# Performance work log

Measured on AMD Instinct MI355X. Metric: run time of the kernel, lower is better.

## Reference

```python
import jax, jax.numpy as jnp
import numpy as np

B, S, I, H = 64, 2048, 128, 256


def setup_inputs() -> dict:
    key = jax.random.key(0)
    ks = jax.random.split(key, 14)
    std = 1.0 / np.sqrt(H)
    def mat(k, shape):
        # xavier-normal-ish init (exact distribution irrelevant for correctness)
        fan_in, fan_out = shape
        s = np.sqrt(2.0 / (fan_in + fan_out))
        return jax.random.normal(k, shape, dtype=jnp.float32) * s
    def vec(k):
        return jax.random.uniform(k, (H,), dtype=jnp.float32, minval=-std, maxval=std)
    return {
        "x": jax.random.normal(ks[0], (B, S, I), dtype=jnp.float32),
        "U_f": mat(ks[1], (I, H)), "W_f": mat(ks[2], (H, H)), "b_f": vec(ks[3]),
        "U_i": mat(ks[4], (I, H)), "W_i": mat(ks[5], (H, H)), "b_i": vec(ks[6]),
        "U_o": mat(ks[7], (I, H)), "W_o": mat(ks[8], (H, H)), "b_o": vec(ks[9]),
        "U_c": mat(ks[10], (I, H)), "W_c": mat(ks[11], (H, H)), "b_c": vec(ks[12]),
    }


def _lstm(x, U_f, W_f, b_f, U_i, W_i, b_i, U_o, W_o, b_o, U_c, W_c, b_c):
    batch, seq, _ = x.shape
    hid = W_f.shape[0]
    # Fuse the 4 input projections into one GEMM over the whole sequence (same math).
    U = jnp.concatenate([U_f, U_i, U_o, U_c], axis=1)           # [I, 4H]
    W = jnp.concatenate([W_f, W_i, W_o, W_c], axis=1)           # [H, 4H]
    b = jnp.concatenate([b_f, b_i, b_o, b_c], axis=0)           # [4H]
    xg = jnp.einsum('bsi,ig->sbg', x, U) + b                    # [S, B, 4H]

    def step(carry, xg_t):
        h, c = carry
        g = xg_t + h @ W                                         # [B, 4H]
        f_t = jax.nn.sigmoid(g[:, 0 * hid:1 * hid])
        i_t = jax.nn.sigmoid(g[:, 1 * hid:2 * hid])
        o_t = jax.nn.sigmoid(g[:, 2 * hid:3 * hid])
        # NOTE: source uses sigmoid (not tanh) for the candidate cell
        c_tilde = jax.nn.sigmoid(g[:, 3 * hid:4 * hid])
        c_new = f_t * c + i_t * c_tilde
        h_new = o_t * jnp.tanh(c_new)
        return (h_new, c_new), h_new

    h0 = jnp.zeros((batch, hid), dtype=x.dtype)
    c0 = jnp.zeros((batch, hid), dtype=x.dtype)
    (h_T, c_T), hs = jax.lax.scan(step, (h0, c0), xg)
    hidden_seq = jnp.transpose(hs, (1, 0, 2))                    # [B, S, H]
    return hidden_seq, (h_T, c_T)


def reference(x, U_f, W_f, b_f, U_i, W_i, b_i, U_o, W_o, b_o, U_c, W_c, b_c):
    return _lstm(x, U_f, W_f, b_f, U_i, W_i, b_i, U_o, W_o, b_o, U_c, W_c, b_c)
```

## Files before the change

### kernel.cpp

```cpp
#include <hip/hip_runtime.h>
#include <stdint.h>

typedef unsigned short ushort_t;
typedef unsigned int uint32;

#define SEQ   2048
#define BATCH 64
#define INDIM 128
#define HID   256
#define NGRP  4
#define NWGG  16
#define HSZ   (BATCH*SEQ*HID)

typedef __attribute__((ext_vector_type(8))) short short8;
typedef __attribute__((ext_vector_type(4))) float float4_t;
typedef __attribute__((ext_vector_type(2))) uint32 uint2_t;

__device__ __forceinline__ ushort_t f2bf(float f) {
  uint32 u = __builtin_bit_cast(uint32, f);
  u += 0x7FFFu + ((u >> 16) & 1u);
  return (ushort_t)(u >> 16);
}
__device__ __forceinline__ float fast_sigmoid(float x) {
  return 1.0f / (1.0f + __expf(-x));
}
__device__ __forceinline__ float fast_tanh(float x) {
  return 1.0f - 2.0f / (__expf(2.0f * x) + 1.0f);
}
template<int CTRL>
__device__ __forceinline__ float bcast_quad(float v) {
  int r = __builtin_amdgcn_mov_dpp(__builtin_bit_cast(int, v), CTRL, 0xF, 0xF, true);
  return __builtin_bit_cast(float, r);
}

__device__ __forceinline__ void load16_bypass(short8& d, const ushort_t* p) {
  asm volatile("global_load_dwordx4 %0, %1, off sc0 sc1"
               : "=v"(d) : "v"(p) : "memory");
}
__device__ __forceinline__ void store_short_bypass(ushort_t* p, uint32 v) {
  asm volatile("global_store_short %0, %1, off sc0 sc1"
               :: "v"(p), "v"(v) : "memory");
}
__device__ __forceinline__ void store_dword_bypass(uint32* p, uint32 v) {
  asm volatile("global_store_dword %0, %1, off sc0 sc1"
               :: "v"(p), "v"(v) : "memory");
}
__device__ __forceinline__ void issue_poll(uint32& v, const uint32* p) {
  asm volatile("global_load_dword %0, %1, off sc0 sc1"
               : "=v"(v) : "v"(p) : "memory");
}
__device__ __forceinline__ void wait_vm1(uint32& v) {
  asm volatile("s_waitcnt vmcnt(1)" : "+v"(v) :: "memory");
}
__device__ __forceinline__ void drain_tied2(uint32& a, uint32& b) {
  asm volatile("s_waitcnt vmcnt(0)" : "+v"(a), "+v"(b) :: "memory");
}
__device__ __forceinline__ void wait8(short8* c) {
  asm volatile("s_waitcnt vmcnt(0)"
               : "+v"(c[0]), "+v"(c[1]), "+v"(c[2]), "+v"(c[3]),
                 "+v"(c[4]), "+v"(c[5]), "+v"(c[6]), "+v"(c[7])
               :: "memory");
}
__device__ __forceinline__ void drain_vm() {
  asm volatile("s_waitcnt vmcnt(0)" ::: "memory");
}

__global__ void pack_init(const float* __restrict__ x,
                          const float* __restrict__ Wf, const float* __restrict__ Wi,
                          const float* __restrict__ Wo, const float* __restrict__ Wc,
                          const float* __restrict__ Uf, const float* __restrict__ Ui,
                          const float* __restrict__ Uo, const float* __restrict__ Uc,
                          const float* __restrict__ bf_, const float* __restrict__ bi_,
                          const float* __restrict__ bo_, const float* __restrict__ bc_,
                          ushort_t* __restrict__ BM2, float* __restrict__ bp2,
                          ushort_t* __restrict__ xbf, uint32* __restrict__ flags) {
  int idx = blockIdx.x * 256 + threadIdx.x;
  {
    int e = idx & 7, lane = (idx >> 3) & 63, q = (idx >> 9) & 3,
        grp = (idx >> 11) & 3, t = idx >> 13;
    if (t < SEQ) {
      int row = grp * 16 + (lane & 15);
      int k = q * 32 + (lane >> 4) * 8 + e;
      xbf[idx] = f2bf(x[(row * SEQ + t) * INDIM + k]);
    }
  }
  if (idx < 64 * 12 * 512) {
    int e = idx & 7, lane = (idx >> 3) & 63;
    int kf = (idx >> 9) % 12, jw = (idx >> 9) / 12;
    int w = jw & 3, j = jw >> 2;
    int llo = lane & 15, lhi = lane >> 4;
    int n = j * 16 + w * 4 + (llo >> 2);
    int g = llo & 3;
    int k = kf * 32 + lhi * 8 + e;
    const float* W4[4] = {Wf, Wi, Wo, Wc};
    const float* U4[4] = {Uf, Ui, Uo, Uc};
    float v = (k < HID) ? W4[g][k * HID + n] : U4[g][(k - HID) * HID + n];
    BM2[idx] = f2bf(v);
  }
  if (idx < 1024) {
    int llo = idx & 15, jw = idx >> 4;
    int w = jw & 3, j = jw >> 2;
    int n = j * 16 + w * 4 + (llo >> 2);
    int g = llo & 3;
    const float* B4[4] = {bf_, bi_, bo_, bc_};
    bp2[idx] = B4[g][n];
  }
  if (idx < NGRP * 64) flags[idx] = 0;
}

__global__ __launch_bounds__(256, 1) void lstm_seq(
    const ushort_t* __restrict__ xbf, const ushort_t* __restrict__ BM2,
    const float* __restrict__ bp2, uint2_t* hpub, uint32* flags,
    float* __restrict__ out)
{
  const int i    = blockIdx.x & 3;
  const int j    = blockIdx.x >> 2;
  const int tid  = threadIdx.x;
  const int wave = tid >> 6;
  const int lane = tid & 63;
  const int lhi  = lane >> 4;
  const int llo  = lane & 15;
  const int Lr   = lane & 3;
  const int csub = llo >> 2;
  const int row  = lhi * 4 + Lr;

  short8 bfrag[12];
  {
    const ushort_t* bsrc = BM2 + (size_t)((j * 4 + wave) * 12) * 512 + lane * 8;
#pragma unroll
    for (int kf = 0; kf < 12; ++kf)
      bfrag[kf] = *(const short8*)(bsrc + kf * 512);
  }
  const float bias = bp2[(j * 4 + wave) * 16 + llo];

  float c_reg[4] = {0.f, 0.f, 0.f, 0.f};
  const int sown = j * 4 + wave;
  const int colg = sown * 4 + csub;
  uint32* myflag = &flags[(i << 6) + sown];
  const uint32* pollp = &flags[(i << 6) + lane];

  short8 xq[4];
  {
    const ushort_t* xs = xbf + (size_t)i * 2048 + lane * 8;
#pragma unroll
    for (int q = 0; q < 4; ++q) xq[q] = *(const short8*)(xs + q * 512);
  }

  for (int t = 0; t < SEQ; ++t) {
    float4_t acc = {bias, bias, bias, bias};
#pragma unroll
    for (int q = 0; q < 4; ++q)
      acc = __builtin_amdgcn_mfma_f32_16x16x32_bf16(xq[q], bfrag[8 + q], acc, 0, 0, 0);
    float4_t accA = {0.f, 0.f, 0.f, 0.f};
    float4_t accB = {0.f, 0.f, 0.f, 0.f};

    if (t > 0) {
      const uint32 want = (uint32)t;
      uint32 va, vb;
      issue_poll(va, pollp);
      issue_poll(vb, pollp);
      for (;;) {
        wait_vm1(va);
        if (__all((int)(va >= want))) break;
        issue_poll(va, pollp);
        wait_vm1(vb);
        if (__all((int)(vb >= want))) break;
        issue_poll(vb, pollp);
      }
      drain_tied2(va, vb);
      const ushort_t* hb = (const ushort_t*)
          (hpub + (size_t)(i * 2 + ((t - 1) & 1)) * 1024);
      short8 hf[8];
#pragma unroll
      for (int kf = 0; kf < 8; ++kf)
        load16_bypass(hf[kf], hb + (((kf * 4 + lhi) * 16 + llo) * 2) * 4);
      wait8(hf);
#pragma unroll
      for (int kf = 0; kf < 4; ++kf) {
        accA = __builtin_amdgcn_mfma_f32_16x16x32_bf16(hf[2 * kf],     bfrag[2 * kf],     accA, 0, 0, 0);
        accB = __builtin_amdgcn_mfma_f32_16x16x32_bf16(hf[2 * kf + 1], bfrag[2 * kf + 1], accB, 0, 0, 0);
      }
    }

    float hv0, hv1, hv2, hv3;
#pragma unroll
    for (int r = 0; r < 4; ++r) {
      float s  = fast_sigmoid(acc[r] + accA[r] + accB[r]);
      float fv = bcast_quad<0x00>(s);
      float iv = bcast_quad<0x55>(s);
      float ov = bcast_quad<0xAA>(s);
      float cv = bcast_quad<0xFF>(s);
      float cn = fv * c_reg[r] + iv * cv;
      c_reg[r] = cn;
      float h  = ov * fast_tanh(cn);
      if      (r == 0) hv0 = h;
      else if (r == 1) hv1 = h;
      else if (r == 2) hv2 = h;
      else             hv3 = h;
    }
    float val = (Lr == 0) ? hv0 : (Lr == 1) ? hv1 : (Lr == 2) ? hv2 : hv3;

    if (t < SEQ - 1) {
      ushort_t* hbo = (ushort_t*)(hpub + (size_t)(i * 2 + (t & 1)) * 1024);
      store_short_bypass(hbo + ((sown >> 1) * 32 + row * 2 + (sown & 1)) * 4 + csub,
                         (uint32)f2bf(val));
      drain_vm();
      if (lane == 0)
        store_dword_bypass(myflag, (uint32)(t + 1));
      out[((size_t)(16 * i + row) * SEQ + t) * HID + colg] = val;
      const ushort_t* xs = xbf + (size_t)((t + 1) * 4 + i) * 2048 + lane * 8;
#pragma unroll
      for (int q = 0; q < 4; ++q) xq[q] = *(const short8*)(xs + q * 512);
    } else {
      out[((size_t)(16 * i + row) * SEQ + t) * HID + colg] = val;
      out[HSZ + (size_t)(16 * i + row) * HID + colg] = val;
      float cva = (Lr == 0) ? c_reg[0] : (Lr == 1) ? c_reg[1]
                : (Lr == 2) ? c_reg[2] : c_reg[3];
      out[HSZ + BATCH * HID + (size_t)(16 * i + row) * HID + colg] = cva;
    }
  }
}

extern "C" void kernel_launch(void* const* d_in, const int* in_sizes, int n_in,
                              void* d_out, int out_size, void* d_ws, size_t ws_size,
                              hipStream_t stream) {
  const float* xp  = (const float*)d_in[0];
  const float* Uf  = (const float*)d_in[1];
  const float* Wf  = (const float*)d_in[2];
  const float* bf_ = (const float*)d_in[3];
  const float* Ui  = (const float*)d_in[4];
  const float* Wi  = (const float*)d_in[5];
  const float* bi_ = (const float*)d_in[6];
  const float* Uo  = (const float*)d_in[7];
  const float* Wo  = (const float*)d_in[8];
  const float* bo_ = (const float*)d_in[9];
  const float* Uc  = (const float*)d_in[10];
  const float* Wc  = (const float*)d_in[11];
  const float* bc_ = (const float*)d_in[12];

  char* ws = (char*)d_ws;
  ushort_t* BM2   = (ushort_t*)(ws);
  float*    bp2   = (float*)(ws + 786432);
  uint2_t*  hpub  = (uint2_t*)(ws + 790528);
  uint32*   flags = (uint32*)(ws + 856064);
  ushort_t* xbf   = (ushort_t*)(ws + 1048576);
  float*    out   = (float*)d_out;

  pack_init<<<65536, 256, 0, stream>>>(xp, Wf, Wi, Wo, Wc, Uf, Ui, Uo, Uc,
                                       bf_, bi_, bo_, bc_, BM2, bp2, xbf, flags);
  lstm_seq<<<NGRP * NWGG, 256, 0, stream>>>(xbf, BM2, bp2, hpub, flags, out);
}
```

Before: 4.636 ms.

## Replace flag polling with step-tagged hidden-state words for inter-block sync

Each published hidden value now carries the timestep in its upper 16 bits as a single dword. Consumers load the whole hidden tile speculatively and check the tags instead of first polling per-producer flags and then loading. This removes the store-drain-flag round trip on the producer side and one dependent load round trip on the consumer side for each timestep. The next x tile is also prefetched earlier with plain loads and a partial vmcnt wait. The cost is twice the bytes of hidden-state traffic, repacking into bf16 before the MFMA, and a fallback polling loop when the tags are stale.

Result: slower. 15.08 ms (+225.3%).

```diff
diff --git a/kernel.cpp b/kernel.cpp
--- a/kernel.cpp
+++ b/kernel.cpp
@@ -14,7 +14,7 @@
 
 typedef __attribute__((ext_vector_type(8))) short short8;
 typedef __attribute__((ext_vector_type(4))) float float4_t;
-typedef __attribute__((ext_vector_type(2))) uint32 uint2_t;
+typedef __attribute__((ext_vector_type(4))) uint32 uint4_t;
 
 __device__ __forceinline__ ushort_t f2bf(float f) {
   uint32 u = __builtin_bit_cast(uint32, f);
@@ -33,13 +33,9 @@
   return __builtin_bit_cast(float, r);
 }
 
-__device__ __forceinline__ void load16_bypass(short8& d, const ushort_t* p) {
+__device__ __forceinline__ void load16_bypass(uint4_t& d, const uint32* p) {
   asm volatile("global_load_dwordx4 %0, %1, off sc0 sc1"
                : "=v"(d) : "v"(p) : "memory");
-}
-__device__ __forceinline__ void store_short_bypass(ushort_t* p, uint32 v) {
-  asm volatile("global_store_short %0, %1, off sc0 sc1"
-               :: "v"(p), "v"(v) : "memory");
 }
 __device__ __forceinline__ void store_dword_bypass(uint32* p, uint32 v) {
   asm volatile("global_store_dword %0, %1, off sc0 sc1"
@@ -55,14 +51,25 @@
 __device__ __forceinline__ void drain_tied2(uint32& a, uint32& b) {
   asm volatile("s_waitcnt vmcnt(0)" : "+v"(a), "+v"(b) :: "memory");
 }
-__device__ __forceinline__ void wait8(short8* c) {
+__device__ __forceinline__ void load16_plain(short8& d, const ushort_t* p) {
+  asm volatile("global_load_dwordx4 %0, %1, off"
+               : "=v"(d) : "v"(p) : "memory");
+}
+__device__ __forceinline__ void wait_xq18(short8* x) {
+  asm volatile("s_waitcnt vmcnt(18)"
+               : "+v"(x[0]), "+v"(x[1]), "+v"(x[2]), "+v"(x[3]) :: "memory");
+}
+__device__ __forceinline__ void wait_xq0(short8* x) {
   asm volatile("s_waitcnt vmcnt(0)"
-               : "+v"(c[0]), "+v"(c[1]), "+v"(c[2]), "+v"(c[3]),
-                 "+v"(c[4]), "+v"(c[5]), "+v"(c[6]), "+v"(c[7])
+               : "+v"(x[0]), "+v"(x[1]), "+v"(x[2]), "+v"(x[3]) :: "memory");
+}
+__device__ __forceinline__ void wait16u(uint4_t* h) {
+  asm volatile("s_waitcnt vmcnt(0)"
+               : "+v"(h[0]),  "+v"(h[1]),  "+v"(h[2]),  "+v"(h[3]),
+                 "+v"(h[4]),  "+v"(h[5]),  "+v"(h[6]),  "+v"(h[7]),
+                 "+v"(h[8]),  "+v"(h[9]),  "+v"(h[10]), "+v"(h[11]),
+                 "+v"(h[12]), "+v"(h[13]), "+v"(h[14]), "+v"(h[15])
                :: "memory");
-}
-__device__ __forceinline__ void drain_vm() {
-  asm volatile("s_waitcnt vmcnt(0)" ::: "memory");
 }
 
 __global__ void pack_init(const float* __restrict__ x,
@@ -73,7 +80,7 @@
                           const float* __restrict__ bf_, const float* __restrict__ bi_,
                           const float* __restrict__ bo_, const float* __restrict__ bc_,
                           ushort_t* __restrict__ BM2, float* __restrict__ bp2,
-                          ushort_t* __restrict__ xbf, uint32* __restrict__ flags) {
+                          ushort_t* __restrict__ xbf, uint32* __restrict__ hpubz) {
   int idx = blockIdx.x * 256 + threadIdx.x;
   {
     int e = idx & 7, lane = (idx >> 3) & 63, q = (idx >> 9) & 3,
@@ -105,13 +112,12 @@
     const float* B4[4] = {bf_, bi_, bo_, bc_};
     bp2[idx] = B4[g][n];
   }
-  if (idx < NGRP * 64) flags[idx] = 0;
+  if (idx < NGRP * 2 * 4096) hpubz[idx] = 0;
 }
 
 __global__ __launch_bounds__(256, 1) void lstm_seq(
     const ushort_t* __restrict__ xbf, const ushort_t* __restrict__ BM2,
-    const float* __restrict__ bp2, uint2_t* hpub, uint32* flags,
-    float* __restrict__ out)
+    const float* __restrict__ bp2, uint32* hpub, float* __restrict__ out)
 {
   const int i    = blockIdx.x & 3;
   const int j    = blockIdx.x >> 2;
@@ -136,17 +142,27 @@
   float c_reg[4] = {0.f, 0.f, 0.f, 0.f};
   const int sown = j * 4 + wave;
   const int colg = sown * 4 + csub;
-  uint32* myflag = &flags[(i << 6) + sown];
-  const uint32* pollp = &flags[(i << 6) + lane];
 
   short8 xq[4];
   {
     const ushort_t* xs = xbf + (size_t)i * 2048 + lane * 8;
 #pragma unroll
-    for (int q = 0; q < 4; ++q) xq[q] = *(const short8*)(xs + q * 512);
+    for (int q = 0; q < 4; ++q) load16_plain(xq[q], xs + q * 512);
+    wait_xq0(xq);
   }
 
   for (int t = 0; t < SEQ; ++t) {
+    uint4_t hd[16];
+    const uint32* cb = hpub + (size_t)(i * 2 + ((t - 1) & 1)) * 4096 + llo * 256;
+    if (t > 0) {
+#pragma unroll
+      for (int f = 0; f < 8; ++f) {
+        load16_bypass(hd[2 * f],     cb + f * 32 + lhi * 8);
+        load16_bypass(hd[2 * f + 1], cb + f * 32 + lhi * 8 + 4);
+      }
+      wait_xq18(xq);
+    }
+
     float4_t acc = {bias, bias, bias, bias};
 #pragma unroll
     for (int q = 0; q < 4; ++q)
@@ -155,31 +171,71 @@
     float4_t accB = {0.f, 0.f, 0.f, 0.f};
 
     if (t > 0) {
-      const uint32 want = (uint32)t;
-      uint32 va, vb;
-      issue_poll(va, pollp);
-      issue_poll(vb, pollp);
-      for (;;) {
-        wait_vm1(va);
-        if (__all((int)(va >= want))) break;
-        issue_poll(va, pollp);
-        wait_vm1(vb);
-        if (__all((int)(vb >= want))) break;
-        issue_poll(vb, pollp);
+      wait16u(hd);
+      const uint32 pat = (uint32)t << 16;
+      uint32 bad = 0;
+#pragma unroll
+      for (int n = 0; n < 16; ++n)
+#pragma unroll
+        for (int c = 0; c < 4; ++c)
+          bad |= (hd[n][c] ^ pat) & 0xFFFF0000u;
+      if (!__all((int)(bad == 0u))) {
+        const uint32* pb = hpub + (size_t)(i * 2 + ((t - 1) & 1)) * 4096 +
+                           ((lane & 15) << 8) + (lane << 2);
+        uint32 va, vb;
+        issue_poll(va, pb);
+        issue_poll(vb, pb);
+        for (;;) {
+          wait_vm1(va);
+          if (__all((int)((va >> 16) >= (uint32)t))) break;
+          issue_poll(va, pb);
+          wait_vm1(vb);
+          if (__all((int)((vb >> 16) >= (uint32)t))) break;
+          issue_poll(vb, pb);
+        }
+        drain_tied2(va, vb);
+        for (;;) {
+#pragma unroll
+          for (int f = 0; f < 8; ++f) {
+            load16_bypass(hd[2 * f],     cb + f * 32 + lhi * 8);
+            load16_bypass(hd[2 * f + 1], cb + f * 32 + lhi * 8 + 4);
+          }
+          wait16u(hd);
+          uint32 bad2 = 0;
+#pragma unroll
+          for (int n = 0; n < 16; ++n)
+#pragma unroll
+            for (int c = 0; c < 4; ++c)
+              bad2 |= (hd[n][c] ^ pat) & 0xFFFF0000u;
+          if (__all((int)(bad2 == 0u))) break;
+          __builtin_amdgcn_s_sleep(1);
+        }
       }
-      drain_tied2(va, vb);
-      const ushort_t* hb = (const ushort_t*)
-          (hpub + (size_t)(i * 2 + ((t - 1) & 1)) * 1024);
-      short8 hf[8];
-#pragma unroll
-      for (int kf = 0; kf < 8; ++kf)
-        load16_bypass(hf[kf], hb + (((kf * 4 + lhi) * 16 + llo) * 2) * 4);
-      wait8(hf);
+      if (t < SEQ - 1) {
+        const ushort_t* xs = xbf + (size_t)((t + 1) * 4 + i) * 2048 + lane * 8;
+#pragma unroll
+        for (int q = 0; q < 4; ++q) load16_plain(xq[q], xs + q * 512);
+      }
 #pragma unroll
       for (int kf = 0; kf < 4; ++kf) {
-        accA = __builtin_amdgcn_mfma_f32_16x16x32_bf16(hf[2 * kf],     bfrag[2 * kf],     accA, 0, 0, 0);
-        accB = __builtin_amdgcn_mfma_f32_16x16x32_bf16(hf[2 * kf + 1], bfrag[2 * kf + 1], accB, 0, 0, 0);
+        uint4_t wA, wB;
+        wA[0] = (hd[4 * kf][0]     & 0xFFFFu) | (hd[4 * kf][1]     << 16);
+        wA[1] = (hd[4 * kf][2]     & 0xFFFFu) | (hd[4 * kf][3]     << 16);
+        wA[2] = (hd[4 * kf + 1][0] & 0xFFFFu) | (hd[4 * kf + 1][1] << 16);
+        wA[3] = (hd[4 * kf + 1][2] & 0xFFFFu) | (hd[4 * kf + 1][3] << 16);
+        wB[0] = (hd[4 * kf + 2][0] & 0xFFFFu) | (hd[4 * kf + 2][1] << 16);
+        wB[1] = (hd[4 * kf + 2][2] & 0xFFFFu) | (hd[4 * kf + 2][3] << 16);
+        wB[2] = (hd[4 * kf + 3][0] & 0xFFFFu) | (hd[4 * kf + 3][1] << 16);
+        wB[3] = (hd[4 * kf + 3][2] & 0xFFFFu) | (hd[4 * kf + 3][3] << 16);
+        accA = __builtin_amdgcn_mfma_f32_16x16x32_bf16(
+                   __builtin_bit_cast(short8, wA), bfrag[2 * kf],     accA, 0, 0, 0);
+        accB = __builtin_amdgcn_mfma_f32_16x16x32_bf16(
+                   __builtin_bit_cast(short8, wB), bfrag[2 * kf + 1], accB, 0, 0, 0);
       }
+    } else {
+      const ushort_t* xs = xbf + (size_t)(1 * 4 + i) * 2048 + lane * 8;
+#pragma unroll
+      for (int q = 0; q < 4; ++q) load16_plain(xq[q], xs + q * 512);
     }
 
     float hv0, hv1, hv2, hv3;
@@ -201,16 +257,10 @@
     float val = (Lr == 0) ? hv0 : (Lr == 1) ? hv1 : (Lr == 2) ? hv2 : hv3;
 
     if (t < SEQ - 1) {
-      ushort_t* hbo = (ushort_t*)(hpub + (size_t)(i * 2 + (t & 1)) * 1024);
-      store_short_bypass(hbo + ((sown >> 1) * 32 + row * 2 + (sown & 1)) * 4 + csub,
-                         (uint32)f2bf(val));
-      drain_vm();
-      if (lane == 0)
-        store_dword_bypass(myflag, (uint32)(t + 1));
+      uint32 pv = (uint32)f2bf(val) | (((uint32)(t + 1)) << 16);
+      store_dword_bypass(hpub + (size_t)(i * 2 + (t & 1)) * 4096 +
+                         row * 256 + colg, pv);
       out[((size_t)(16 * i + row) * SEQ + t) * HID + colg] = val;
-      const ushort_t* xs = xbf + (size_t)((t + 1) * 4 + i) * 2048 + lane * 8;
-#pragma unroll
-      for (int q = 0; q < 4; ++q) xq[q] = *(const short8*)(xs + q * 512);
     } else {
       out[((size_t)(16 * i + row) * SEQ + t) * HID + colg] = val;
       out[HSZ + (size_t)(16 * i + row) * HID + colg] = val;
@@ -241,12 +291,11 @@
   char* ws = (char*)d_ws;
   ushort_t* BM2   = (ushort_t*)(ws);
   float*    bp2   = (float*)(ws + 786432);
-  uint2_t*  hpub  = (uint2_t*)(ws + 790528);
-  uint32*   flags = (uint32*)(ws + 856064);
+  uint32*   hpub  = (uint32*)(ws + 790528);
   ushort_t* xbf   = (ushort_t*)(ws + 1048576);
   float*    out   = (float*)d_out;
 
   pack_init<<<65536, 256, 0, stream>>>(xp, Wf, Wi, Wo, Wc, Uf, Ui, Uo, Uc,
-                                       bf_, bi_, bo_, bc_, BM2, bp2, xbf, flags);
-  lstm_seq<<<NGRP * NWGG, 256, 0, stream>>>(xbf, BM2, bp2, hpub, flags, out);
-}
+                                       bf_, bi_, bo_, bc_, BM2, bp2, xbf, hpub);
+  lstm_seq<<<NGRP * NWGG, 256, 0, stream>>>(xbf, BM2, bp2, hpub, out);
+}
```
